# Kernel optimization log

Hardware: AMD Instinct MI355X
Metric: run time of the kernel (lower is better)

The kernel has to match this reference:

```python
import jax, jax.numpy as jnp
import numpy as np

TANH_CONST = 2.5
TEMPERATURE = 5.0


def setup_inputs() -> dict:
    key = jax.random.key(0)
    ks = jax.random.split(key, 9)
    B, L, NB, H, NC = 16384, 64, 8, 128, 1000
    return {
        "class_ids": jax.random.randint(ks[0], (B,), 0, NC),
        "gumbel_u": jax.random.uniform(ks[1], (L, B, NB), dtype=jnp.float32),
        "g_emb": jax.random.normal(ks[2], (NC, H), dtype=jnp.float32) * 0.1,
        "w_emb": jax.random.normal(ks[3], (NB, H), dtype=jnp.float32) * 0.1,
        "w_soft": jax.random.normal(ks[4], (NB, H), dtype=jnp.float32) * 0.1,
        "w_ih": jax.random.normal(ks[5], (4 * H, H), dtype=jnp.float32) * 0.1,
        "w_hh": jax.random.normal(ks[6], (4 * H, H), dtype=jnp.float32) * 0.1,
        "b_ih": jax.random.normal(ks[7], (4 * H,), dtype=jnp.float32) * 0.1,
        "b_hh": jax.random.normal(ks[8], (4 * H,), dtype=jnp.float32) * 0.1,
    }


def reference(class_ids, gumbel_u, g_emb, w_emb, w_soft, w_ih, w_hh, b_ih, b_hh):
    B = class_ids.shape[0]
    H = g_emb.shape[1]
    x0 = g_emb[class_ids]                      # [B, H] class embedding (reused each step)
    h0 = jnp.zeros((B, H), x0.dtype)
    c0 = jnp.zeros((B, H), x0.dtype)

    def step(carry, u):
        h, c, x = carry
        gates = x @ w_ih.T + h @ w_hh.T + b_ih + b_hh   # [B, 4H], torch gate order i,f,g,o
        i, f, g, o = jnp.split(gates, 4, axis=-1)
        c2 = jax.nn.sigmoid(f) * c + jax.nn.sigmoid(i) * jnp.tanh(g)
        h2 = jax.nn.sigmoid(o) * jnp.tanh(c2)
        logit = h2 @ w_soft.T                           # [B, NB]
        logit = TANH_CONST * jnp.tanh(logit / TEMPERATURE)
        # categorical sample via gumbel-max
        uc = jnp.clip(u, 1e-8, 1.0 - 1e-8)
        gmb = -jnp.log(-jnp.log(uc))
        branch = jnp.argmax(logit + gmb, axis=-1)       # [B] int
        logp = jax.nn.log_softmax(logit, axis=-1)
        lp = jnp.take_along_axis(logp, branch[:, None], axis=1)[:, 0]
        ent = -jnp.sum(jnp.exp(logp) * logp, axis=-1)
        x2 = (w_emb[branch] + x0) * 0.5
        return (h2, c2, x2), (branch, lp, ent)

    _, (arcs, lps, ents) = jax.lax.scan(step, (h0, c0, x0), gumbel_u)
    # stack along dim=1 like torch.stack(..., dim=1) -> [B, L]
    sample_arc = arcs.T
    sample_log_prob = lps.T
    sample_entropy = ents.T
    sample_prob = jnp.exp(sample_log_prob)
    return sample_arc, sample_log_prob, sample_entropy, sample_prob
```

## Files before the change

### kernel.cpp

```cpp
#include <hip/hip_runtime.h>
#include <math.h>

#define HD 128
#define NBR 8
#define LSTEPS 64
#define TILE_B 32
#define HT_PAD 36
#define HRM_PAD 132
#define WS_PAD 132

#define WPT_OFF   0
#define WIPT_OFF  65536
#define PP_OFF    131072
#define BSUM_OFF  135168

__global__ __launch_bounds__(256) void setup_kernel(
    const float* __restrict__ w_emb, const float* __restrict__ w_ih,
    const float* __restrict__ w_hh, const float* __restrict__ b_ih,
    const float* __restrict__ b_hh, float* __restrict__ ws)
{
  int tid = blockIdx.x * blockDim.x + threadIdx.x;
  if (tid < 65536) {
    int k = tid >> 9, col = tid & 511;
    int hh = col >> 2, q = col & 3;
    ws[WPT_OFF + tid]  = w_hh[(q*HD + hh)*HD + k];
    ws[WIPT_OFF + tid] = w_ih[(q*HD + hh)*HD + k];
  }
  if (tid < 4096) {
    int j = tid >> 9, rem = tid & 511;
    int q = rem >> 7, hh2 = rem & 127;
    const float* wr = w_ih + (q*HD + hh2)*HD;
    const float* er = w_emb + j*HD;
    float s = 0.f;
    for (int k = 0; k < HD; ++k) s = fmaf(er[k], wr[k], s);
    ws[PP_OFF + (size_t)j*512 + 4*hh2 + q] = s + b_ih[q*HD + hh2] + b_hh[q*HD + hh2];
  }
  if (tid < 512) {
    int q = tid >> 7, hh2 = tid & 127;
    ws[BSUM_OFF + tid] = b_ih[q*HD + hh2] + b_hh[q*HD + hh2];
  }
}

__device__ __forceinline__ float fsig(float x) {
  return __fdividef(1.f, 1.f + __expf(-x));
}
__device__ __forceinline__ float ftanh(float x) {
  float ax = fabsf(x);
  float e  = __expf(-2.f * ax);
  float r  = __fdividef(1.f - e, 1.f + e);
  return copysignf(r, x);
}

#define ROWQ16(qi, wq, H0, H1, H2, H3) \
  acc[qi][0]  = fmaf((H0).x, wq, acc[qi][0]);  acc[qi][1]  = fmaf((H0).y, wq, acc[qi][1]);  \
  acc[qi][2]  = fmaf((H0).z, wq, acc[qi][2]);  acc[qi][3]  = fmaf((H0).w, wq, acc[qi][3]);  \
  acc[qi][4]  = fmaf((H1).x, wq, acc[qi][4]);  acc[qi][5]  = fmaf((H1).y, wq, acc[qi][5]);  \
  acc[qi][6]  = fmaf((H1).z, wq, acc[qi][6]);  acc[qi][7]  = fmaf((H1).w, wq, acc[qi][7]);  \
  acc[qi][8]  = fmaf((H2).x, wq, acc[qi][8]);  acc[qi][9]  = fmaf((H2).y, wq, acc[qi][9]);  \
  acc[qi][10] = fmaf((H2).z, wq, acc[qi][10]); acc[qi][11] = fmaf((H2).w, wq, acc[qi][11]); \
  acc[qi][12] = fmaf((H3).x, wq, acc[qi][12]); acc[qi][13] = fmaf((H3).y, wq, acc[qi][13]); \
  acc[qi][14] = fmaf((H3).z, wq, acc[qi][14]); acc[qi][15] = fmaf((H3).w, wq, acc[qi][15]);

#define KFMA16(W, H0, H1, H2, H3) \
  ROWQ16(0, (W).x, H0, H1, H2, H3) ROWQ16(1, (W).y, H0, H1, H2, H3) \
  ROWQ16(2, (W).z, H0, H1, H2, H3) ROWQ16(3, (W).w, H0, H1, H2, H3)

#define BAR_LGKM() asm volatile("s_waitcnt lgkmcnt(0)\n\ts_barrier" ::: "memory")

__global__ __launch_bounds__(256, 2) void ctrl_kernel(
    const int* __restrict__ class_ids,
    const float* __restrict__ gumbel_u,
    const float* __restrict__ g_emb,
    const float* __restrict__ w_soft,
    const float* __restrict__ ws,
    float* __restrict__ out,
    int Btot)
{
  __shared__ __align__(16) float hT[HD * HT_PAD];
  __shared__ __align__(16) float h_rm[TILE_B * HRM_PAD];
  __shared__ __align__(16) float wsoft_l[NBR * WS_PAD];
  __shared__ __align__(16) float pp_l[NBR * 512];
  __shared__ int br_l[TILE_B];

  const int tid = threadIdx.x;
  const int b0  = blockIdx.x * TILE_B;
  const size_t BL = (size_t)Btot * LSTEPS;

  const float* __restrict__ wpT  = ws + WPT_OFF;
  const float* __restrict__ wipT = ws + WIPT_OFF;

  {
    int col = tid & 127, half = tid >> 7;
    #pragma unroll
    for (int rr = 0; rr < 4; ++rr)
      wsoft_l[(half*4 + rr)*WS_PAD + col] = w_soft[(half*4 + rr)*HD + col];
  }
  for (int i = tid; i < NBR*512; i += 256) pp_l[i] = ws[PP_OFF + i];

  const int hh = tid & 127;
  const int bg = tid >> 7;
  const int sg = tid >> 3;
  const int sr = tid & 7;

  {
    int sb = tid >> 3;
    int kc = tid & 7;
    int cid = class_ids[b0 + sb];
    const float* src = g_emb + (size_t)cid * HD + kc*16;
    #pragma unroll
    for (int ii = 0; ii < 4; ++ii) {
      float4 v = *(const float4*)(src + 4*ii);
      int kb = kc*16 + 4*ii;
      hT[(kb+0)*HT_PAD + sb] = v.x;
      hT[(kb+1)*HT_PAD + sb] = v.y;
      hT[(kb+2)*HT_PAD + sb] = v.z;
      hT[(kb+3)*HT_PAD + sb] = v.w;
    }
  }
  __syncthreads();

  float q0[4][16];
  {
    float acc[4][16];
    #pragma unroll
    for (int q = 0; q < 4; ++q)
      #pragma unroll
      for (int j = 0; j < 16; ++j) acc[q][j] = 0.f;

    const float* wr = wipT + 4*hh;
    const float* hr = hT + bg*16;
    #pragma unroll 2
    for (int k = 0; k < HD; ++k) {
      float4 w  = *(const float4*)(wr);
      float4 h0 = *(const float4*)(hr);
      float4 h1 = *(const float4*)(hr + 4);
      float4 h2 = *(const float4*)(hr + 8);
      float4 h3 = *(const float4*)(hr + 12);
      KFMA16(w, h0, h1, h2, h3);
      wr += 512; hr += HT_PAD;
    }
    #pragma unroll
    for (int q = 0; q < 4; ++q) {
      float bs = ws[BSUM_OFF + q*HD + hh];
      #pragma unroll
      for (int j = 0; j < 16; ++j)
        q0[q][j] = 0.5f * (acc[q][j] + bs);
    }
  }
  __syncthreads();

  float c[16];
  #pragma unroll
  for (int j = 0; j < 16; ++j) c[j] = 0.f;

  for (int t = 0; t < LSTEPS; ++t) {
    float uval = gumbel_u[((size_t)t * Btot + b0) * NBR + tid];

    float acc[4][16];
    #pragma unroll
    for (int q = 0; q < 4; ++q)
      #pragma unroll
      for (int j = 0; j < 16; ++j) acc[q][j] = q0[q][j];

    if (t > 0) {
      __builtin_amdgcn_s_setprio(1);
      const float* wr = wpT + 4*hh;
      const float* hr = hT + bg*16;
      float4 w0 = *(const float4*)(wr);
      float4 w1 = *(const float4*)(wr + 512);
      float4 hA0 = *(const float4*)(hr);
      float4 hA1 = *(const float4*)(hr + 4);
      float4 hA2 = *(const float4*)(hr + 8);
      float4 hA3 = *(const float4*)(hr + 12);
      #pragma unroll 1
      for (int i = 0; i < 63; ++i) {
        float4 hB0 = *(const float4*)(hr + HT_PAD);
        float4 hB1 = *(const float4*)(hr + HT_PAD + 4);
        float4 hB2 = *(const float4*)(hr + HT_PAD + 8);
        float4 hB3 = *(const float4*)(hr + HT_PAD + 12);
        float4 wn0 = *(const float4*)(wr + 2*512);
        float4 wc0 = w0;
        KFMA16(wc0, hA0, hA1, hA2, hA3);
        float4 hN0 = *(const float4*)(hr + 2*HT_PAD);
        float4 hN1 = *(const float4*)(hr + 2*HT_PAD + 4);
        float4 hN2 = *(const float4*)(hr + 2*HT_PAD + 8);
        float4 hN3 = *(const float4*)(hr + 2*HT_PAD + 12);
        float4 wn1 = *(const float4*)(wr + 3*512);
        float4 wc1 = w1;
        KFMA16(wc1, hB0, hB1, hB2, hB3);
        w0 = wn0; w1 = wn1;
        hA0 = hN0; hA1 = hN1; hA2 = hN2; hA3 = hN3;
        wr += 1024; hr += 2*HT_PAD;
      }
      {
        float4 hB0 = *(const float4*)(hr + HT_PAD);
        float4 hB1 = *(const float4*)(hr + HT_PAD + 4);
        float4 hB2 = *(const float4*)(hr + HT_PAD + 8);
        float4 hB3 = *(const float4*)(hr + HT_PAD + 12);
        KFMA16(w0, hA0, hA1, hA2, hA3);
        KFMA16(w1, hB0, hB1, hB2, hB3);
      }
      __builtin_amdgcn_s_setprio(0);
    }

    BAR_LGKM();

    float h2v[16];
    #pragma unroll
    for (int j = 0; j < 16; ++j) {
      float gi, gf, gg, go;
      if (t == 0) {
        gi = 2.f*acc[0][j]; gf = 2.f*acc[1][j];
        gg = 2.f*acc[2][j]; go = 2.f*acc[3][j];
      } else {
        int br = br_l[bg*16 + j];
        float4 pv = *(const float4*)(&pp_l[br*512 + 4*hh]);
        gi = fmaf(0.5f, pv.x, acc[0][j]);
        gf = fmaf(0.5f, pv.y, acc[1][j]);
        gg = fmaf(0.5f, pv.z, acc[2][j]);
        go = fmaf(0.5f, pv.w, acc[3][j]);
      }
      float iv = fsig(gi);
      float fv = fsig(gf);
      float gv = ftanh(gg);
      float ov = fsig(go);
      float c2 = fmaf(fv, c[j], iv*gv);
      c[j] = c2;
      h2v[j] = ov * ftanh(c2);
    }

    {
      float* dst = &hT[hh*HT_PAD + bg*16];
      *(float4*)(dst)    = make_float4(h2v[0], h2v[1], h2v[2], h2v[3]);
      *(float4*)(dst+4)  = make_float4(h2v[4], h2v[5], h2v[6], h2v[7]);
      *(float4*)(dst+8)  = make_float4(h2v[8], h2v[9], h2v[10],h2v[11]);
      *(float4*)(dst+12) = make_float4(h2v[12],h2v[13],h2v[14],h2v[15]);
      #pragma unroll
      for (int j = 0; j < 16; ++j)
        h_rm[(bg*16 + j)*HRM_PAD + hh] = h2v[j];
    }
    BAR_LGKM();

    {
      const float* hp  = h_rm + sg*HRM_PAD;
      const float* wp2 = wsoft_l + sr*WS_PAD;
      float p = 0.f;
      #pragma unroll
      for (int i = 0; i < 32; ++i) {
        float4 hv = *(const float4*)(hp + 4*i);
        float4 wv = *(const float4*)(wp2 + 4*i);
        p = fmaf(hv.x, wv.x, p); p = fmaf(hv.y, wv.y, p);
        p = fmaf(hv.z, wv.z, p); p = fmaf(hv.w, wv.w, p);
      }
      float lg = 2.5f * ftanh(p * 0.2f);
      float uc = fminf(fmaxf(uval, 1e-8f), 0.99999999f);
      float y  = lg - __logf(-__logf(uc));
      int   bi = sr;
      float by = y;
      #pragma unroll
      for (int mk = 1; mk < 8; mk <<= 1) {
        float oy = __shfl_xor(by, mk, 64);
        int   ob = __shfl_xor(bi, mk, 64);
        if (oy > by || (oy == by && ob < bi)) { by = oy; bi = ob; }
      }
      float m = lg;
      #pragma unroll
      for (int mk = 1; mk < 8; mk <<= 1) m = fmaxf(m, __shfl_xor(m, mk, 64));
      float se = __expf(lg - m);
      #pragma unroll
      for (int mk = 1; mk < 8; mk <<= 1) se += __shfl_xor(se, mk, 64);
      float lse = __logf(se);
      float lpi = (lg - m) - lse;
      float ent = __expf(lpi) * lpi;
      #pragma unroll
      for (int mk = 1; mk < 8; mk <<= 1) ent += __shfl_xor(ent, mk, 64);
      ent = -ent;
      float lgbr = __shfl(lg, (tid & 56) + bi, 64);
      float lp = (lgbr - m) - lse;
      if (sr == 0) {
        br_l[sg] = bi;
        size_t row = (size_t)(b0 + sg) * LSTEPS + t;
        out[row]        = (float)bi;
        out[BL + row]   = lp;
        out[2*BL + row] = ent;
        out[3*BL + row] = __expf(lp);
      }
    }
  }
}

extern "C" void kernel_launch(void* const* d_in, const int* in_sizes, int n_in,
                              void* d_out, int out_size, void* d_ws, size_t ws_size,
                              hipStream_t stream) {
  const int*   class_ids = (const int*)d_in[0];
  const float* gumbel_u  = (const float*)d_in[1];
  const float* g_emb     = (const float*)d_in[2];
  const float* w_emb     = (const float*)d_in[3];
  const float* w_soft    = (const float*)d_in[4];
  const float* w_ih      = (const float*)d_in[5];
  const float* w_hh      = (const float*)d_in[6];
  const float* b_ih      = (const float*)d_in[7];
  const float* b_hh      = (const float*)d_in[8];
  float* out = (float*)d_out;
  float* ws  = (float*)d_ws;
  int B = in_sizes[0];

  hipLaunchKernelGGL(setup_kernel, dim3(256), dim3(256), 0, stream,
                     w_emb, w_ih, w_hh, b_ih, b_hh, ws);
  hipLaunchKernelGGL(ctrl_kernel, dim3(B / TILE_B), dim3(256), 0, stream,
                     class_ids, gumbel_u, g_emb, w_soft, ws, out, B);
}
```

Baseline: 1.943 ms.

## Halve batch tile to 16 rows and raise occupancy to four blocks per CU

Shrinks the per-block batch tile from 32 to 16, so each thread holds 8 rather than 16 batch accumulators per gate, and raises launch bounds to 4 blocks per multiprocessor. The per-branch projection table moves out of shared memory and is read from global memory, which shrinks LDS so more blocks fit. The softmax/sampling stage now runs on only half the threads. The aim is more resident waves to hide latency across the serial recurrence. The cost is twice as many blocks each streaming the full recurrent weight matrix, so weight traffic per useful FMA doubles, and the table gathers now go through global memory.

```diff
diff --git a/kernel.cpp b/kernel.cpp
--- a/kernel.cpp
+++ b/kernel.cpp
@@ -4,8 +4,8 @@
 #define HD 128
 #define NBR 8
 #define LSTEPS 64
-#define TILE_B 32
-#define HT_PAD 36
+#define TILE_B 16
+#define HT_PAD 20
 #define HRM_PAD 132
 #define WS_PAD 132
 
@@ -51,23 +51,19 @@
   return copysignf(r, x);
 }
 
-#define ROWQ16(qi, wq, H0, H1, H2, H3) \
-  acc[qi][0]  = fmaf((H0).x, wq, acc[qi][0]);  acc[qi][1]  = fmaf((H0).y, wq, acc[qi][1]);  \
-  acc[qi][2]  = fmaf((H0).z, wq, acc[qi][2]);  acc[qi][3]  = fmaf((H0).w, wq, acc[qi][3]);  \
-  acc[qi][4]  = fmaf((H1).x, wq, acc[qi][4]);  acc[qi][5]  = fmaf((H1).y, wq, acc[qi][5]);  \
-  acc[qi][6]  = fmaf((H1).z, wq, acc[qi][6]);  acc[qi][7]  = fmaf((H1).w, wq, acc[qi][7]);  \
-  acc[qi][8]  = fmaf((H2).x, wq, acc[qi][8]);  acc[qi][9]  = fmaf((H2).y, wq, acc[qi][9]);  \
-  acc[qi][10] = fmaf((H2).z, wq, acc[qi][10]); acc[qi][11] = fmaf((H2).w, wq, acc[qi][11]); \
-  acc[qi][12] = fmaf((H3).x, wq, acc[qi][12]); acc[qi][13] = fmaf((H3).y, wq, acc[qi][13]); \
-  acc[qi][14] = fmaf((H3).z, wq, acc[qi][14]); acc[qi][15] = fmaf((H3).w, wq, acc[qi][15]);
-
-#define KFMA16(W, H0, H1, H2, H3) \
-  ROWQ16(0, (W).x, H0, H1, H2, H3) ROWQ16(1, (W).y, H0, H1, H2, H3) \
-  ROWQ16(2, (W).z, H0, H1, H2, H3) ROWQ16(3, (W).w, H0, H1, H2, H3)
+#define ROWQ8(qi, wq, H0, H1) \
+  acc[qi][0] = fmaf((H0).x, wq, acc[qi][0]); acc[qi][1] = fmaf((H0).y, wq, acc[qi][1]); \
+  acc[qi][2] = fmaf((H0).z, wq, acc[qi][2]); acc[qi][3] = fmaf((H0).w, wq, acc[qi][3]); \
+  acc[qi][4] = fmaf((H1).x, wq, acc[qi][4]); acc[qi][5] = fmaf((H1).y, wq, acc[qi][5]); \
+  acc[qi][6] = fmaf((H1).z, wq, acc[qi][6]); acc[qi][7] = fmaf((H1).w, wq, acc[qi][7]);
+
+#define KFMA8(W, H0, H1) \
+  ROWQ8(0, (W).x, H0, H1) ROWQ8(1, (W).y, H0, H1) \
+  ROWQ8(2, (W).z, H0, H1) ROWQ8(3, (W).w, H0, H1)
 
 #define BAR_LGKM() asm volatile("s_waitcnt lgkmcnt(0)\n\ts_barrier" ::: "memory")
 
-__global__ __launch_bounds__(256, 2) void ctrl_kernel(
+__global__ __launch_bounds__(256, 4) void ctrl_kernel(
     const int* __restrict__ class_ids,
     const float* __restrict__ gumbel_u,
     const float* __restrict__ g_emb,
@@ -79,7 +75,6 @@
   __shared__ __align__(16) float hT[HD * HT_PAD];
   __shared__ __align__(16) float h_rm[TILE_B * HRM_PAD];
   __shared__ __align__(16) float wsoft_l[NBR * WS_PAD];
-  __shared__ __align__(16) float pp_l[NBR * 512];
   __shared__ int br_l[TILE_B];
 
   const int tid = threadIdx.x;
@@ -88,6 +83,7 @@
 
   const float* __restrict__ wpT  = ws + WPT_OFF;
   const float* __restrict__ wipT = ws + WIPT_OFF;
+  const float* __restrict__ ppg  = ws + PP_OFF;
 
   {
     int col = tid & 127, half = tid >> 7;
@@ -95,126 +91,118 @@
     for (int rr = 0; rr < 4; ++rr)
       wsoft_l[(half*4 + rr)*WS_PAD + col] = w_soft[(half*4 + rr)*HD + col];
   }
-  for (int i = tid; i < NBR*512; i += 256) pp_l[i] = ws[PP_OFF + i];
 
   const int hh = tid & 127;
   const int bg = tid >> 7;
-  const int sg = tid >> 3;
+  const int sg = (tid >> 3) & 15;
   const int sr = tid & 7;
 
   {
-    int sb = tid >> 3;
-    int kc = tid & 7;
+    int sb = tid >> 4;
+    int kc = tid & 15;
     int cid = class_ids[b0 + sb];
-    const float* src = g_emb + (size_t)cid * HD + kc*16;
-    #pragma unroll
-    for (int ii = 0; ii < 4; ++ii) {
-      float4 v = *(const float4*)(src + 4*ii);
-      int kb = kc*16 + 4*ii;
-      hT[(kb+0)*HT_PAD + sb] = v.x;
-      hT[(kb+1)*HT_PAD + sb] = v.y;
-      hT[(kb+2)*HT_PAD + sb] = v.z;
-      hT[(kb+3)*HT_PAD + sb] = v.w;
-    }
+    const float* src = g_emb + (size_t)cid * HD + kc*8;
+    float4 v0 = *(const float4*)(src);
+    float4 v1 = *(const float4*)(src + 4);
+    int kb = kc*8;
+    hT[(kb+0)*HT_PAD + sb] = v0.x;
+    hT[(kb+1)*HT_PAD + sb] = v0.y;
+    hT[(kb+2)*HT_PAD + sb] = v0.z;
+    hT[(kb+3)*HT_PAD + sb] = v0.w;
+    hT[(kb+4)*HT_PAD + sb] = v1.x;
+    hT[(kb+5)*HT_PAD + sb] = v1.y;
+    hT[(kb+6)*HT_PAD + sb] = v1.z;
+    hT[(kb+7)*HT_PAD + sb] = v1.w;
   }
   __syncthreads();
 
-  float q0[4][16];
+  float q0[4][8];
   {
-    float acc[4][16];
+    float acc[4][8];
     #pragma unroll
     for (int q = 0; q < 4; ++q)
       #pragma unroll
-      for (int j = 0; j < 16; ++j) acc[q][j] = 0.f;
+      for (int j = 0; j < 8; ++j) acc[q][j] = 0.f;
 
     const float* wr = wipT + 4*hh;
-    const float* hr = hT + bg*16;
+    const float* hr = hT + bg*8;
     #pragma unroll 2
     for (int k = 0; k < HD; ++k) {
       float4 w  = *(const float4*)(wr);
       float4 h0 = *(const float4*)(hr);
       float4 h1 = *(const float4*)(hr + 4);
-      float4 h2 = *(const float4*)(hr + 8);
-      float4 h3 = *(const float4*)(hr + 12);
-      KFMA16(w, h0, h1, h2, h3);
+      KFMA8(w, h0, h1);
       wr += 512; hr += HT_PAD;
     }
     #pragma unroll
     for (int q = 0; q < 4; ++q) {
       float bs = ws[BSUM_OFF + q*HD + hh];
       #pragma unroll
-      for (int j = 0; j < 16; ++j)
+      for (int j = 0; j < 8; ++j)
         q0[q][j] = 0.5f * (acc[q][j] + bs);
     }
   }
   __syncthreads();
 
-  float c[16];
+  float c[8];
   #pragma unroll
-  for (int j = 0; j < 16; ++j) c[j] = 0.f;
+  for (int j = 0; j < 8; ++j) c[j] = 0.f;
 
   for (int t = 0; t < LSTEPS; ++t) {
-    float uval = gumbel_u[((size_t)t * Btot + b0) * NBR + tid];
-
-    float acc[4][16];
+    float uval = 0.f;
+    if (tid < 128) uval = gumbel_u[((size_t)t * Btot + b0) * NBR + tid];
+
+    float acc[4][8];
     #pragma unroll
     for (int q = 0; q < 4; ++q)
       #pragma unroll
-      for (int j = 0; j < 16; ++j) acc[q][j] = q0[q][j];
+      for (int j = 0; j < 8; ++j) acc[q][j] = q0[q][j];
 
     if (t > 0) {
       __builtin_amdgcn_s_setprio(1);
       const float* wr = wpT + 4*hh;
-      const float* hr = hT + bg*16;
+      const float* hr = hT + bg*8;
       float4 w0 = *(const float4*)(wr);
       float4 w1 = *(const float4*)(wr + 512);
       float4 hA0 = *(const float4*)(hr);
       float4 hA1 = *(const float4*)(hr + 4);
-      float4 hA2 = *(const float4*)(hr + 8);
-      float4 hA3 = *(const float4*)(hr + 12);
-      #pragma unroll 1
+      #pragma unroll 2
       for (int i = 0; i < 63; ++i) {
         float4 hB0 = *(const float4*)(hr + HT_PAD);
         float4 hB1 = *(const float4*)(hr + HT_PAD + 4);
-        float4 hB2 = *(const float4*)(hr + HT_PAD + 8);
-        float4 hB3 = *(const float4*)(hr + HT_PAD + 12);
         float4 wn0 = *(const float4*)(wr + 2*512);
         float4 wc0 = w0;
-        KFMA16(wc0, hA0, hA1, hA2, hA3);
+        KFMA8(wc0, hA0, hA1);
         float4 hN0 = *(const float4*)(hr + 2*HT_PAD);
         float4 hN1 = *(const float4*)(hr + 2*HT_PAD + 4);
-        float4 hN2 = *(const float4*)(hr + 2*HT_PAD + 8);
-        float4 hN3 = *(const float4*)(hr + 2*HT_PAD + 12);
         float4 wn1 = *(const float4*)(wr + 3*512);
         float4 wc1 = w1;
-        KFMA16(wc1, hB0, hB1, hB2, hB3);
+        KFMA8(wc1, hB0, hB1);
         w0 = wn0; w1 = wn1;
-        hA0 = hN0; hA1 = hN1; hA2 = hN2; hA3 = hN3;
+        hA0 = hN0; hA1 = hN1;
         wr += 1024; hr += 2*HT_PAD;
       }
       {
         float4 hB0 = *(const float4*)(hr + HT_PAD);
         float4 hB1 = *(const float4*)(hr + HT_PAD + 4);
-        float4 hB2 = *(const float4*)(hr + HT_PAD + 8);
-        float4 hB3 = *(const float4*)(hr + HT_PAD + 12);
-        KFMA16(w0, hA0, hA1, hA2, hA3);
-        KFMA16(w1, hB0, hB1, hB2, hB3);
+        KFMA8(w0, hA0, hA1);
+        KFMA8(w1, hB0, hB1);
       }
       __builtin_amdgcn_s_setprio(0);
     }
 
     BAR_LGKM();
 
-    float h2v[16];
-    #pragma unroll
-    for (int j = 0; j < 16; ++j) {
+    float h2v[8];
+    #pragma unroll
+    for (int j = 0; j < 8; ++j) {
       float gi, gf, gg, go;
       if (t == 0) {
         gi = 2.f*acc[0][j]; gf = 2.f*acc[1][j];
         gg = 2.f*acc[2][j]; go = 2.f*acc[3][j];
       } else {
-        int br = br_l[bg*16 + j];
-        float4 pv = *(const float4*)(&pp_l[br*512 + 4*hh]);
+        int br = br_l[bg*8 + j];
+        float4 pv = *(const float4*)(ppg + (size_t)br*512 + 4*hh);
         gi = fmaf(0.5f, pv.x, acc[0][j]);
         gf = fmaf(0.5f, pv.y, acc[1][j]);
         gg = fmaf(0.5f, pv.z, acc[2][j]);
@@ -230,18 +218,16 @@
     }
 
     {
-      float* dst = &hT[hh*HT_PAD + bg*16];
-      *(float4*)(dst)    = make_float4(h2v[0], h2v[1], h2v[2], h2v[3]);
-      *(float4*)(dst+4)  = make_float4(h2v[4], h2v[5], h2v[6], h2v[7]);
-      *(float4*)(dst+8)  = make_float4(h2v[8], h2v[9], h2v[10],h2v[11]);
-      *(float4*)(dst+12) = make_float4(h2v[12],h2v[13],h2v[14],h2v[15]);
-      #pragma unroll
-      for (int j = 0; j < 16; ++j)
-        h_rm[(bg*16 + j)*HRM_PAD + hh] = h2v[j];
+      float* dst = &hT[hh*HT_PAD + bg*8];
+      *(float4*)(dst)   = make_float4(h2v[0], h2v[1], h2v[2], h2v[3]);
+      *(float4*)(dst+4) = make_float4(h2v[4], h2v[5], h2v[6], h2v[7]);
+      #pragma unroll
+      for (int j = 0; j < 8; ++j)
+        h_rm[(bg*8 + j)*HRM_PAD + hh] = h2v[j];
     }
     BAR_LGKM();
 
-    {
+    if (tid < 128) {
       const float* hp  = h_rm + sg*HRM_PAD;
       const float* wp2 = wsoft_l + sr*WS_PAD;
       float p = 0.f;
```

After: 2.372 ms. 22.1% more time.

## Restructure recurrent matvec loop to prefetch weights only and relax launch bounds

Applied to the files above, without the earlier changes.

The inner recurrent GEMV loop no longer software-pipelines the LDS hidden-state loads in registers. It now loads h rows inline per k and double-buffers only the weight float4s, unrolled four k-steps per iteration. Launch bounds change from 2 blocks to 1 block per SM minimum, which lets the compiler use more registers. The aim is to cut register pressure and spills and to give the scheduler more freedom. The cost is possibly lower occupancy and exposed LDS latency.

```diff
diff --git a/kernel.cpp b/kernel.cpp
--- a/kernel.cpp
+++ b/kernel.cpp
@@ -51,23 +51,48 @@
   return copysignf(r, x);
 }
 
-#define ROWQ16(qi, wq, H0, H1, H2, H3) \
-  acc[qi][0]  = fmaf((H0).x, wq, acc[qi][0]);  acc[qi][1]  = fmaf((H0).y, wq, acc[qi][1]);  \
-  acc[qi][2]  = fmaf((H0).z, wq, acc[qi][2]);  acc[qi][3]  = fmaf((H0).w, wq, acc[qi][3]);  \
-  acc[qi][4]  = fmaf((H1).x, wq, acc[qi][4]);  acc[qi][5]  = fmaf((H1).y, wq, acc[qi][5]);  \
-  acc[qi][6]  = fmaf((H1).z, wq, acc[qi][6]);  acc[qi][7]  = fmaf((H1).w, wq, acc[qi][7]);  \
-  acc[qi][8]  = fmaf((H2).x, wq, acc[qi][8]);  acc[qi][9]  = fmaf((H2).y, wq, acc[qi][9]);  \
-  acc[qi][10] = fmaf((H2).z, wq, acc[qi][10]); acc[qi][11] = fmaf((H2).w, wq, acc[qi][11]); \
-  acc[qi][12] = fmaf((H3).x, wq, acc[qi][12]); acc[qi][13] = fmaf((H3).y, wq, acc[qi][13]); \
-  acc[qi][14] = fmaf((H3).z, wq, acc[qi][14]); acc[qi][15] = fmaf((H3).w, wq, acc[qi][15]);
-
-#define KFMA16(W, H0, H1, H2, H3) \
-  ROWQ16(0, (W).x, H0, H1, H2, H3) ROWQ16(1, (W).y, H0, H1, H2, H3) \
-  ROWQ16(2, (W).z, H0, H1, H2, H3) ROWQ16(3, (W).w, H0, H1, H2, H3)
+#define KFMA16L(W, HPTR) do { \
+    float4 h0 = *(const float4*)(HPTR); \
+    float4 h1 = *(const float4*)((HPTR) + 4); \
+    float4 h2 = *(const float4*)((HPTR) + 8); \
+    float4 h3 = *(const float4*)((HPTR) + 12); \
+    acc[0][0]  = fmaf(h0.x, (W).x, acc[0][0]);  acc[0][1]  = fmaf(h0.y, (W).x, acc[0][1]);  \
+    acc[0][2]  = fmaf(h0.z, (W).x, acc[0][2]);  acc[0][3]  = fmaf(h0.w, (W).x, acc[0][3]);  \
+    acc[0][4]  = fmaf(h1.x, (W).x, acc[0][4]);  acc[0][5]  = fmaf(h1.y, (W).x, acc[0][5]);  \
+    acc[0][6]  = fmaf(h1.z, (W).x, acc[0][6]);  acc[0][7]  = fmaf(h1.w, (W).x, acc[0][7]);  \
+    acc[0][8]  = fmaf(h2.x, (W).x, acc[0][8]);  acc[0][9]  = fmaf(h2.y, (W).x, acc[0][9]);  \
+    acc[0][10] = fmaf(h2.z, (W).x, acc[0][10]); acc[0][11] = fmaf(h2.w, (W).x, acc[0][11]); \
+    acc[0][12] = fmaf(h3.x, (W).x, acc[0][12]); acc[0][13] = fmaf(h3.y, (W).x, acc[0][13]); \
+    acc[0][14] = fmaf(h3.z, (W).x, acc[0][14]); acc[0][15] = fmaf(h3.w, (W).x, acc[0][15]); \
+    acc[1][0]  = fmaf(h0.x, (W).y, acc[1][0]);  acc[1][1]  = fmaf(h0.y, (W).y, acc[1][1]);  \
+    acc[1][2]  = fmaf(h0.z, (W).y, acc[1][2]);  acc[1][3]  = fmaf(h0.w, (W).y, acc[1][3]);  \
+    acc[1][4]  = fmaf(h1.x, (W).y, acc[1][4]);  acc[1][5]  = fmaf(h1.y, (W).y, acc[1][5]);  \
+    acc[1][6]  = fmaf(h1.z, (W).y, acc[1][6]);  acc[1][7]  = fmaf(h1.w, (W).y, acc[1][7]);  \
+    acc[1][8]  = fmaf(h2.x, (W).y, acc[1][8]);  acc[1][9]  = fmaf(h2.y, (W).y, acc[1][9]);  \
+    acc[1][10] = fmaf(h2.z, (W).y, acc[1][10]); acc[1][11] = fmaf(h2.w, (W).y, acc[1][11]); \
+    acc[1][12] = fmaf(h3.x, (W).y, acc[1][12]); acc[1][13] = fmaf(h3.y, (W).y, acc[1][13]); \
+    acc[1][14] = fmaf(h3.z, (W).y, acc[1][14]); acc[1][15] = fmaf(h3.w, (W).y, acc[1][15]); \
+    acc[2][0]  = fmaf(h0.x, (W).z, acc[2][0]);  acc[2][1]  = fmaf(h0.y, (W).z, acc[2][1]);  \
+    acc[2][2]  = fmaf(h0.z, (W).z, acc[2][2]);  acc[2][3]  = fmaf(h0.w, (W).z, acc[2][3]);  \
+    acc[2][4]  = fmaf(h1.x, (W).z, acc[2][4]);  acc[2][5]  = fmaf(h1.y, (W).z, acc[2][5]);  \
+    acc[2][6]  = fmaf(h1.z, (W).z, acc[2][6]);  acc[2][7]  = fmaf(h1.w, (W).z, acc[2][7]);  \
+    acc[2][8]  = fmaf(h2.x, (W).z, acc[2][8]);  acc[2][9]  = fmaf(h2.y, (W).z, acc[2][9]);  \
+    acc[2][10] = fmaf(h2.z, (W).z, acc[2][10]); acc[2][11] = fmaf(h2.w, (W).z, acc[2][11]); \
+    acc[2][12] = fmaf(h3.x, (W).z, acc[2][12]); acc[2][13] = fmaf(h3.y, (W).z, acc[2][13]); \
+    acc[2][14] = fmaf(h3.z, (W).z, acc[2][14]); acc[2][15] = fmaf(h3.w, (W).z, acc[2][15]); \
+    acc[3][0]  = fmaf(h0.x, (W).w, acc[3][0]);  acc[3][1]  = fmaf(h0.y, (W).w, acc[3][1]);  \
+    acc[3][2]  = fmaf(h0.z, (W).w, acc[3][2]);  acc[3][3]  = fmaf(h0.w, (W).w, acc[3][3]);  \
+    acc[3][4]  = fmaf(h1.x, (W).w, acc[3][4]);  acc[3][5]  = fmaf(h1.y, (W).w, acc[3][5]);  \
+    acc[3][6]  = fmaf(h1.z, (W).w, acc[3][6]);  acc[3][7]  = fmaf(h1.w, (W).w, acc[3][7]);  \
+    acc[3][8]  = fmaf(h2.x, (W).w, acc[3][8]);  acc[3][9]  = fmaf(h2.y, (W).w, acc[3][9]);  \
+    acc[3][10] = fmaf(h2.z, (W).w, acc[3][10]); acc[3][11] = fmaf(h2.w, (W).w, acc[3][11]); \
+    acc[3][12] = fmaf(h3.x, (W).w, acc[3][12]); acc[3][13] = fmaf(h3.y, (W).w, acc[3][13]); \
+    acc[3][14] = fmaf(h3.z, (W).w, acc[3][14]); acc[3][15] = fmaf(h3.w, (W).w, acc[3][15]); \
+  } while (0)
 
 #define BAR_LGKM() asm volatile("s_waitcnt lgkmcnt(0)\n\ts_barrier" ::: "memory")
 
-__global__ __launch_bounds__(256, 2) void ctrl_kernel(
+__global__ __launch_bounds__(256, 1) void ctrl_kernel(
     const int* __restrict__ class_ids,
     const float* __restrict__ gumbel_u,
     const float* __restrict__ g_emb,
@@ -131,12 +156,8 @@
     const float* hr = hT + bg*16;
     #pragma unroll 2
     for (int k = 0; k < HD; ++k) {
-      float4 w  = *(const float4*)(wr);
-      float4 h0 = *(const float4*)(hr);
-      float4 h1 = *(const float4*)(hr + 4);
-      float4 h2 = *(const float4*)(hr + 8);
-      float4 h3 = *(const float4*)(hr + 12);
-      KFMA16(w, h0, h1, h2, h3);
+      float4 w = *(const float4*)(wr);
+      KFMA16L(w, hr);
       wr += 512; hr += HT_PAD;
     }
     #pragma unroll
@@ -166,39 +187,27 @@
       __builtin_amdgcn_s_setprio(1);
       const float* wr = wpT + 4*hh;
       const float* hr = hT + bg*16;
-      float4 w0 = *(const float4*)(wr);
-      float4 w1 = *(const float4*)(wr + 512);
-      float4 hA0 = *(const float4*)(hr);
-      float4 hA1 = *(const float4*)(hr + 4);
-      float4 hA2 = *(const float4*)(hr + 8);
-      float4 hA3 = *(const float4*)(hr + 12);
+      float4 wX0 = *(const float4*)(wr);
+      float4 wX1 = *(const float4*)(wr + 512);
       #pragma unroll 1
-      for (int i = 0; i < 63; ++i) {
-        float4 hB0 = *(const float4*)(hr + HT_PAD);
-        float4 hB1 = *(const float4*)(hr + HT_PAD + 4);
-        float4 hB2 = *(const float4*)(hr + HT_PAD + 8);
-        float4 hB3 = *(const float4*)(hr + HT_PAD + 12);
-        float4 wn0 = *(const float4*)(wr + 2*512);
-        float4 wc0 = w0;
-        KFMA16(wc0, hA0, hA1, hA2, hA3);
-        float4 hN0 = *(const float4*)(hr + 2*HT_PAD);
-        float4 hN1 = *(const float4*)(hr + 2*HT_PAD + 4);
-        float4 hN2 = *(const float4*)(hr + 2*HT_PAD + 8);
-        float4 hN3 = *(const float4*)(hr + 2*HT_PAD + 12);
-        float4 wn1 = *(const float4*)(wr + 3*512);
-        float4 wc1 = w1;
-        KFMA16(wc1, hB0, hB1, hB2, hB3);
-        w0 = wn0; w1 = wn1;
-        hA0 = hN0; hA1 = hN1; hA2 = hN2; hA3 = hN3;
-        wr += 1024; hr += 2*HT_PAD;
+      for (int i = 0; i < 31; ++i) {
+        float4 wY0 = *(const float4*)(wr + 2*512);
+        float4 wY1 = *(const float4*)(wr + 3*512);
+        KFMA16L(wX0, hr);
+        KFMA16L(wX1, hr + HT_PAD);
+        wX0 = *(const float4*)(wr + 4*512);
+        wX1 = *(const float4*)(wr + 5*512);
+        KFMA16L(wY0, hr + 2*HT_PAD);
+        KFMA16L(wY1, hr + 3*HT_PAD);
+        wr += 4*512; hr += 4*HT_PAD;
       }
       {
-        float4 hB0 = *(const float4*)(hr + HT_PAD);
-        float4 hB1 = *(const float4*)(hr + HT_PAD + 4);
-        float4 hB2 = *(const float4*)(hr + HT_PAD + 8);
-        float4 hB3 = *(const float4*)(hr + HT_PAD + 12);
-        KFMA16(w0, hA0, hA1, hA2, hA3);
-        KFMA16(w1, hB0, hB1, hB2, hB3);
+        float4 wY0 = *(const float4*)(wr + 2*512);
+        float4 wY1 = *(const float4*)(wr + 3*512);
+        KFMA16L(wX0, hr);
+        KFMA16L(wX1, hr + HT_PAD);
+        KFMA16L(wY0, hr + 2*HT_PAD);
+        KFMA16L(wY1, hr + 3*HT_PAD);
       }
       __builtin_amdgcn_s_setprio(0);
     }
```

Measured after the change: 2.469 ms. 27.1% more time.
